# Kernel tuning notes

Hardware: AMD Instinct MI355X
Metric: run time of the kernel (lower is better)

The kernel has to match this reference:

```python
import jax, jax.numpy as jnp
import numpy as np

N, C, H, W = 64, 512, 16, 16
MEM_DIM, NUM_CLS = 2000, 10


def setup_inputs() -> dict:
    key = jax.random.key(0)
    k1, k2, k3 = jax.random.split(key, 3)
    z = jax.random.normal(k1, (N, C, H, W), dtype=jnp.float32)
    cls = jax.random.randint(k2, (N,), 0, NUM_CLS, dtype=jnp.int32)
    # nn.init.normal_(memory, 0.0, 0.02)
    memory = 0.02 * jax.random.normal(k3, (1, C, MEM_DIM, NUM_CLS), dtype=jnp.float32)
    return {"z": z, "cls": cls, "memory": memory}


def reference(z, cls, memory):
    n, c, h, w_ = z.shape
    hw = h * w_
    # memory[0,:,:,cls] -> (C, M, N) -> per-sample class memory (N, C, M)
    mem_cls = jnp.transpose(memory[0][:, :, cls], (2, 0, 1))  # (N, C, M)
    zf = z.reshape(n, c, hw)  # (N, C, HW)
    # similarity = -||z - m||^2 = 2 z.m - ||z||^2 - ||m||^2
    zm = jnp.einsum('ncp,ncm->npm', zf, mem_cls)          # (N, HW, M)
    z2 = jnp.sum(zf * zf, axis=1)[:, :, None]             # (N, HW, 1)
    m2 = jnp.sum(mem_cls * mem_cls, axis=1)[:, None, :]   # (N, 1, M)
    sim = 2.0 * zm - z2 - m2                               # (N, HW, M)
    log_w = jax.nn.log_softmax(sim, axis=2)
    w = jax.nn.softmax(sim, axis=2)
    w_hat = w  # topk == -1 in forward path
    # z_hat = bmm(mem_cls (N,C,M), w_hat^T (N,M,HW)) -> (N,C,HW)
    z_hat = jnp.einsum('ncm,npm->ncp', mem_cls, w_hat).reshape(n, c, h, w_)
    return (z_hat, w_hat, w, log_w)
```

## Files before the change

### kernel.cpp

```cpp
#include <hip/hip_runtime.h>
#include <hip/hip_bf16.h>
#include <math.h>

#define N_   64
#define C_   512
#define HW_  256
#define M_   2000
#define KCLS 10
#define MP_  2048

typedef __attribute__((ext_vector_type(8))) short bf16x8;
typedef __attribute__((ext_vector_type(4))) float f32x4;

__device__ __forceinline__ short f2bf(float x) {
    __hip_bfloat16 b = __float2bfloat16(x);
    return *reinterpret_cast<short*>(&b);
}
__device__ __forceinline__ float bf2f(short s) {
    __hip_bfloat16 b = *reinterpret_cast<__hip_bfloat16*>(&s);
    return __bfloat162float(b);
}

__global__ __launch_bounds__(256) void gather_mem(const float* __restrict__ mem,
                                                  short* __restrict__ mcm,
                                                  short* __restrict__ mmc) {
    const int m0 = blockIdx.x * 32;
    const int c0 = blockIdx.y * 64;
    __shared__ short tile[KCLS][32][66];
    const int t = threadIdx.x;
    const int mm = t & 31;
    const int m = m0 + mm;
    const int cbase = t >> 5;
    for (int ci = 0; ci < 8; ++ci) {
        const int cl = cbase + ci * 8;
        const int c = c0 + cl;
        short v[KCLS];
        if (m < M_) {
            const float* src = mem + ((size_t)c * M_ + m) * KCLS;
#pragma unroll
            for (int k = 0; k < KCLS; ++k) v[k] = f2bf(src[k]);
        } else {
#pragma unroll
            for (int k = 0; k < KCLS; ++k) v[k] = 0;
        }
#pragma unroll
        for (int k = 0; k < KCLS; ++k) {
            mcm[(size_t)k * (C_ * MP_) + (size_t)c * MP_ + m0 + mm] = v[k];
            tile[k][mm][cl] = v[k];
        }
    }
    __syncthreads();
    const int cc = t & 63;
    const int rbase = t >> 6;
    for (int k = 0; k < KCLS; ++k) {
#pragma unroll
        for (int r = 0; r < 8; ++r) {
            const int mm2 = r * 4 + rbase;
            mmc[(size_t)k * (MP_ * C_) + (size_t)(m0 + mm2) * C_ + c0 + cc] = tile[k][mm2][cc];
        }
    }
}

__global__ __launch_bounds__(256) void transpose_z(const float* __restrict__ z,
                                                   short* __restrict__ zTb) {
    const int c0 = blockIdx.x * 64;
    const int p0 = blockIdx.y * 64;
    const int n = blockIdx.z;
    const float* zp = z + (size_t)n * C_ * HW_;
    __shared__ short tile[64][70];
    const int t = threadIdx.x;
    const int pp = t & 63;
    const int cb = t >> 6;
#pragma unroll
    for (int i = 0; i < 16; ++i) {
        const int cl = i * 4 + cb;
        tile[cl][pp] = f2bf(zp[(size_t)(c0 + cl) * HW_ + p0 + pp]);
    }
    __syncthreads();
    short* dst = zTb + (size_t)n * HW_ * C_;
    const int cc = t & 63;
    const int pb = t >> 6;
#pragma unroll
    for (int i = 0; i < 16; ++i) {
        const int pl = i * 4 + pb;
        dst[(size_t)(p0 + pl) * C_ + c0 + cc] = tile[cc][pl];
    }
}

__global__ __launch_bounds__(256) void m2_kernel(const short* __restrict__ mcm,
                                                 float* __restrict__ m2) {
    const int m = blockIdx.x * 256 + threadIdx.x;
    const int k = blockIdx.y;
    if (m >= M_) return;
    const short* B = mcm + (size_t)k * C_ * MP_;
    float s = 0.f;
    for (int c = 0; c < C_; ++c) {
        float v = bf2f(B[(size_t)c * MP_ + m]);
        s = fmaf(v, v, s);
    }
    m2[k * M_ + m] = s;
}

template<int MODE>
__global__ __launch_bounds__(256) void gemm_nt(const short* __restrict__ Ab,
                                               const short* __restrict__ Bb,
                                               const float* __restrict__ Bf,
                                               const int* __restrict__ cls,
                                               const float* __restrict__ m2,
                                               float* __restrict__ Db) {
    constexpr int K  = (MODE == 0) ? C_ : MP_;
    constexpr int SA = (MODE == 0) ? C_ : MP_;
    constexpr int SB = (MODE == 0) ? C_ : MP_;
    const int bx = blockIdx.x, by = blockIdx.y, n = blockIdx.z;
    const int kc = cls[n];
    const int rowA0 = by * 128, colB0 = bx * 128;

    const short* A;
    const short* B  = nullptr;
    const float* BF = nullptr;
    float* D;
    if constexpr (MODE == 0) {
        A = Ab + (size_t)n * HW_ * C_;
        B = Bb + (size_t)kc * MP_ * C_;
        D = Db + (size_t)n * HW_ * M_;
    } else if constexpr (MODE == 1) {
        A = Ab + (size_t)kc * C_ * MP_;
        BF = Bf + (size_t)n * HW_ * M_;
        D = Db + (size_t)n * C_ * HW_;
    } else {
        A = Ab + (size_t)kc * C_ * MP_;
        B = Bb + (size_t)n * HW_ * MP_;
        D = Db + (size_t)n * C_ * HW_;
    }

    __shared__ short As[128 * 64];
    __shared__ short Bs[128 * 64];

    const int tid = threadIdx.x;
    const int w = tid >> 6, lane = tid & 63;
    const int wr = w >> 1, wc = w & 1;
    const int srow = lane >> 3, sslot = lane & 7;

    f32x4 acc[4][4];
#pragma unroll
    for (int i = 0; i < 4; ++i)
#pragma unroll
        for (int j = 0; j < 4; ++j) acc[i][j] = (f32x4){0.f, 0.f, 0.f, 0.f};

    for (int k0 = 0; k0 < K; k0 += 64) {
#pragma unroll
        for (int i = 0; i < 4; ++i) {
            const int row = w * 32 + i * 8 + srow;
            const int chunk = sslot ^ (row & 7);
            const short* src = A + (size_t)(rowA0 + row) * SA + k0 + chunk * 8;
            __builtin_amdgcn_global_load_lds(
                (const __attribute__((address_space(1))) void*)src,
                (__attribute__((address_space(3))) void*)&As[(w * 32 + i * 8) * 64],
                16, 0, 0);
        }
        if constexpr (MODE != 1) {
#pragma unroll
            for (int i = 0; i < 4; ++i) {
                const int row = w * 32 + i * 8 + srow;
                const int chunk = sslot ^ (row & 7);
                const short* src = B + (size_t)(colB0 + row) * SB + k0 + chunk * 8;
                __builtin_amdgcn_global_load_lds(
                    (const __attribute__((address_space(1))) void*)src,
                    (__attribute__((address_space(3))) void*)&Bs[(w * 32 + i * 8) * 64],
                    16, 0, 0);
            }
        } else {
#pragma unroll
            for (int i = 0; i < 4; ++i) {
                const int row = w * 32 + i * 8 + srow;
                const int kg = k0 + sslot * 8;
                float4 v0 = {0.f, 0.f, 0.f, 0.f}, v1 = {0.f, 0.f, 0.f, 0.f};
                if (kg < M_) {
                    const float* s = BF + (size_t)(colB0 + row) * M_ + kg;
                    v0 = *reinterpret_cast<const float4*>(s);
                    v1 = *reinterpret_cast<const float4*>(s + 4);
                }
                bf16x8 bv;
                bv[0] = f2bf(v0.x); bv[1] = f2bf(v0.y); bv[2] = f2bf(v0.z); bv[3] = f2bf(v0.w);
                bv[4] = f2bf(v1.x); bv[5] = f2bf(v1.y); bv[6] = f2bf(v1.z); bv[7] = f2bf(v1.w);
                *reinterpret_cast<bf16x8*>(&Bs[row * 64 + (sslot ^ (row & 7)) * 8]) = bv;
            }
        }
        __syncthreads();
        bf16x8 a[4][2], b[4][2];
#pragma unroll
        for (int i = 0; i < 4; ++i)
#pragma unroll
            for (int kk = 0; kk < 2; ++kk) {
                const int ra = wr * 64 + i * 16 + (lane & 15);
                const int slot = kk * 4 + (lane >> 4);
                a[i][kk] = *reinterpret_cast<const bf16x8*>(&As[ra * 64 + (slot ^ (ra & 7)) * 8]);
                const int rb = wc * 64 + i * 16 + (lane & 15);
                b[i][kk] = *reinterpret_cast<const bf16x8*>(&Bs[rb * 64 + (slot ^ (rb & 7)) * 8]);
            }
#pragma unroll
        for (int i = 0; i < 4; ++i)
#pragma unroll
            for (int j = 0; j < 4; ++j)
#pragma unroll
                for (int kk = 0; kk < 2; ++kk)
                    acc[i][j] = __builtin_amdgcn_mfma_f32_16x16x32_bf16(a[i][kk], b[j][kk], acc[i][j], 0, 0, 0);
        __syncthreads();
    }

    if constexpr (MODE == 0) {
#pragma unroll
        for (int j = 0; j < 4; ++j) {
            const int col = colB0 + wc * 64 + j * 16 + (lane & 15);
            if (col < M_) {
                const float m2v = m2[kc * M_ + col];
#pragma unroll
                for (int i = 0; i < 4; ++i) {
                    const int row = rowA0 + wr * 64 + i * 16 + (lane >> 4) * 4;
#pragma unroll
                    for (int r = 0; r < 4; ++r)
                        D[(size_t)(row + r) * M_ + col] = 2.f * acc[i][j][r] - m2v;
                }
            }
        }
    } else {
#pragma unroll
        for (int i = 0; i < 4; ++i) {
            const int row = rowA0 + wr * 64 + i * 16 + (lane >> 4) * 4;
#pragma unroll
            for (int j = 0; j < 4; ++j) {
                const int col = colB0 + wc * 64 + j * 16 + (lane & 15);
#pragma unroll
                for (int r = 0; r < 4; ++r)
                    D[(size_t)(row + r) * HW_ + col] = acc[i][j][r];
            }
        }
    }
}

__global__ __launch_bounds__(256) void softmax_kernel(const float* __restrict__ simbuf,
                                                      float* __restrict__ w_hat,
                                                      float* __restrict__ w,
                                                      float* __restrict__ logw,
                                                      short* __restrict__ wb,
                                                      int write_hat) {
    const int r = blockIdx.x;
    const float* srow = simbuf + (size_t)r * M_;
    const int t = threadIdx.x;

    float s0[8];
    float lmax = -INFINITY;
#pragma unroll
    for (int i = 0; i < 8; ++i) {
        int idx = t + i * 256;
        float x = (idx < M_) ? srow[idx] : -INFINITY;
        s0[i] = x;
        lmax = fmaxf(lmax, x);
    }
#pragma unroll
    for (int off = 32; off >= 1; off >>= 1)
        lmax = fmaxf(lmax, __shfl_xor(lmax, off));

    __shared__ float wred[4];
    __shared__ float wsum[4];
    const int wid = t >> 6, lane = t & 63;
    if (lane == 0) wred[wid] = lmax;
    __syncthreads();
    const float gmax = fmaxf(fmaxf(wred[0], wred[1]), fmaxf(wred[2], wred[3]));

    float e[8];
    float lsum = 0.f;
#pragma unroll
    for (int i = 0; i < 8; ++i) {
        int idx = t + i * 256;
        if (idx < M_) {
            e[i] = __expf(s0[i] - gmax);
            lsum += e[i];
        }
    }
#pragma unroll
    for (int off = 32; off >= 1; off >>= 1)
        lsum += __shfl_xor(lsum, off);
    if (lane == 0) wsum[wid] = lsum;
    __syncthreads();
    const float gsum = wsum[0] + wsum[1] + wsum[2] + wsum[3];
    const float inv = 1.f / gsum;
    const float lg  = __logf(gsum);

    size_t base = (size_t)r * M_;
    size_t base2 = (size_t)r * MP_;
#pragma unroll
    for (int i = 0; i < 8; ++i) {
        int idx = t + i * 256;
        if (idx < M_) {
            float wv = e[i] * inv;
            w[base + idx] = wv;
            if (write_hat) w_hat[base + idx] = wv;
            logw[base + idx] = (s0[i] - gmax) - lg;
            if (wb) wb[base2 + idx] = f2bf(wv);
        } else {
            if (wb) wb[base2 + idx] = 0;
        }
    }
}

__global__ __launch_bounds__(256) void copy_kernel(const float* __restrict__ src,
                                                   float* __restrict__ dst, int n4) {
    int i = blockIdx.x * 256 + threadIdx.x;
    int stride = gridDim.x * 256;
    for (; i < n4; i += stride)
        reinterpret_cast<float4*>(dst)[i] = reinterpret_cast<const float4*>(src)[i];
}

extern "C" void kernel_launch(void* const* d_in, const int* in_sizes, int n_in,
                              void* d_out, int out_size, void* d_ws, size_t ws_size,
                              hipStream_t stream) {
    const float* z      = (const float*)d_in[0];
    const int*   cls    = (const int*)d_in[1];
    const float* memory = (const float*)d_in[2];

    float* out   = (float*)d_out;
    float* z_hat = out;
    float* w_hat = z_hat + (size_t)N_ * C_ * HW_;
    float* w     = w_hat + (size_t)N_ * HW_ * M_;
    float* logw  = w     + (size_t)N_ * HW_ * M_;

    const size_t mcm_sh = (size_t)KCLS * C_ * MP_;
    const size_t mmc_sh = mcm_sh;
    const size_t zTb_sh = (size_t)N_ * HW_ * C_;
    const size_t wb_sh  = (size_t)N_ * HW_ * MP_;
    const size_t m2_fl  = (size_t)KCLS * M_;
    const size_t need_base = (mcm_sh + mmc_sh + zTb_sh) * 2 + m2_fl * 4;
    const size_t need_full = need_base + wb_sh * 2;

    short *mcm, *mmc, *zTb, *wb = nullptr;
    float* m2;
    int write_hat;
    if (ws_size >= need_base) {
        char* p = (char*)d_ws;
        mcm = (short*)p;          p += mcm_sh * 2;
        mmc = (short*)p;          p += mmc_sh * 2;
        m2  = (float*)p;          p += m2_fl * 4;
        zTb = (short*)p;          p += zTb_sh * 2;
        if (ws_size >= need_full) wb = (short*)p;
        write_hat = 1;
    } else {
        char* p = (char*)w_hat;
        mcm = (short*)p;          p += mcm_sh * 2;
        mmc = (short*)p;          p += mmc_sh * 2;
        m2  = (float*)p;
        zTb = (short*)z_hat;
        write_hat = 0;
    }
    float* simbuf = logw;

    gather_mem<<<dim3(MP_ / 32, C_ / 64), 256, 0, stream>>>(memory, mcm, mmc);
    transpose_z<<<dim3(C_ / 64, HW_ / 64, N_), 256, 0, stream>>>(z, zTb);
    m2_kernel<<<dim3(MP_ / 256, KCLS), 256, 0, stream>>>(mcm, m2);
    gemm_nt<0><<<dim3(MP_ / 128, HW_ / 128, N_), 256, 0, stream>>>(zTb, mmc, nullptr, cls, m2, simbuf);
    softmax_kernel<<<N_ * HW_, 256, 0, stream>>>(simbuf, w_hat, w, logw, wb, write_hat);
    if (wb)
        gemm_nt<2><<<dim3(HW_ / 128, C_ / 128, N_), 256, 0, stream>>>(mcm, wb, nullptr, cls, m2, z_hat);
    else
        gemm_nt<1><<<dim3(HW_ / 128, C_ / 128, N_), 256, 0, stream>>>(mcm, nullptr, w, cls, m2, z_hat);
    if (!write_hat)
        copy_kernel<<<2048, 256, 0, stream>>>(w, w_hat, (N_ * HW_ * M_) / 4);
}
```

Baseline: 308.4 us.

## Store similarity as bf16 via LDS-staged coalesced epilogues, remap blocks across XCDs

The similarity GEMM now writes its output as bf16 into a padded buffer (row stride 4000 shorts) through an LDS-staged, swizzled tile, so stores are 16-byte and coalesced. The softmax reads one 8-wide bf16 vector per thread and writes w, w_hat and log_w with float4 stores. The z_hat GEMM epilogue is also staged through LDS for float4 stores, and workgroups are remapped so consecutive logical tiles are spread across the 8 XCDs. This halves similarity traffic and removes scattered stores, at the cost of bf16 rounding of the logits before softmax and log_softmax, which may hurt accuracy.

After: 280.3 us. -9.1%, faster.

```diff
diff --git a/kernel.cpp b/kernel.cpp
--- a/kernel.cpp
+++ b/kernel.cpp
@@ -8,6 +8,7 @@
 #define M_   2000
 #define KCLS 10
 #define MP_  2048
+#define SIMS 4000
 
 typedef __attribute__((ext_vector_type(8))) short bf16x8;
 typedef __attribute__((ext_vector_type(4))) float f32x4;
@@ -91,14 +92,13 @@
                                                  float* __restrict__ m2) {
     const int m = blockIdx.x * 256 + threadIdx.x;
     const int k = blockIdx.y;
-    if (m >= M_) return;
     const short* B = mcm + (size_t)k * C_ * MP_;
     float s = 0.f;
     for (int c = 0; c < C_; ++c) {
         float v = bf2f(B[(size_t)c * MP_ + m]);
         s = fmaf(v, v, s);
     }
-    m2[k * M_ + m] = s;
+    m2[k * MP_ + m] = s;
 }
 
 template<int MODE>
@@ -111,30 +111,37 @@
     constexpr int K  = (MODE == 0) ? C_ : MP_;
     constexpr int SA = (MODE == 0) ? C_ : MP_;
     constexpr int SB = (MODE == 0) ? C_ : MP_;
-    const int bx = blockIdx.x, by = blockIdx.y, n = blockIdx.z;
+    constexpr int GX = (MODE == 0) ? 16 : 2;
+    constexpr int GY = (MODE == 0) ? 2 : 4;
+    constexpr int NWG = GX * GY * N_;
+    constexpr int CPX = NWG / 8;
+
+    const int flat = blockIdx.x + GX * (blockIdx.y + GY * blockIdx.z);
+    const int logical = (flat & 7) * CPX + (flat >> 3);
+    const int n  = logical / (GX * GY);
+    const int rr = logical % (GX * GY);
+    const int by = rr / GX, bx = rr % GX;
+
     const int kc = cls[n];
     const int rowA0 = by * 128, colB0 = bx * 128;
 
     const short* A;
     const short* B  = nullptr;
     const float* BF = nullptr;
-    float* D;
     if constexpr (MODE == 0) {
         A = Ab + (size_t)n * HW_ * C_;
         B = Bb + (size_t)kc * MP_ * C_;
-        D = Db + (size_t)n * HW_ * M_;
     } else if constexpr (MODE == 1) {
         A = Ab + (size_t)kc * C_ * MP_;
         BF = Bf + (size_t)n * HW_ * M_;
-        D = Db + (size_t)n * C_ * HW_;
     } else {
         A = Ab + (size_t)kc * C_ * MP_;
         B = Bb + (size_t)n * HW_ * MP_;
-        D = Db + (size_t)n * C_ * HW_;
-    }
-
-    __shared__ short As[128 * 64];
-    __shared__ short Bs[128 * 64];
+    }
+
+    __shared__ short smem[2 * 128 * 64];
+    short* As = smem;
+    short* Bs = smem + 128 * 64;
 
     const int tid = threadIdx.x;
     const int w = tid >> 6, lane = tid & 63;
@@ -209,54 +216,87 @@
     }
 
     if constexpr (MODE == 0) {
-#pragma unroll
-        for (int j = 0; j < 4; ++j) {
-            const int col = colB0 + wc * 64 + j * 16 + (lane & 15);
-            if (col < M_) {
-                const float m2v = m2[kc * M_ + col];
-#pragma unroll
-                for (int i = 0; i < 4; ++i) {
-                    const int row = rowA0 + wr * 64 + i * 16 + (lane >> 4) * 4;
-#pragma unroll
-                    for (int r = 0; r < 4; ++r)
-                        D[(size_t)(row + r) * M_ + col] = 2.f * acc[i][j][r] - m2v;
+        short* outs = smem;
+#pragma unroll
+        for (int i = 0; i < 4; ++i)
+#pragma unroll
+            for (int j = 0; j < 4; ++j) {
+                const int col = wc * 64 + j * 16 + (lane & 15);
+                const float m2v = m2[kc * MP_ + colB0 + col];
+#pragma unroll
+                for (int r = 0; r < 4; ++r) {
+                    const int row = wr * 64 + i * 16 + (lane >> 4) * 4 + r;
+                    outs[row * 128 + (col ^ (((row >> 2) & 7) << 3))] =
+                        f2bf(2.f * acc[i][j][r] - m2v);
                 }
             }
+        __syncthreads();
+        short* Ds = (short*)Db;
+        const size_t rbase = (size_t)n * HW_ + rowA0;
+#pragma unroll
+        for (int it = 0; it < 8; ++it) {
+            const int chunk = tid + it * 256;
+            const int row = chunk >> 4, c8 = (chunk & 15) * 8;
+            bf16x8 v = *reinterpret_cast<const bf16x8*>(
+                &outs[row * 128 + (c8 ^ (((row >> 2) & 7) << 3))]);
+            *reinterpret_cast<bf16x8*>(Ds + (rbase + row) * SIMS + colB0 + c8) = v;
         }
     } else {
-#pragma unroll
-        for (int i = 0; i < 4; ++i) {
-            const int row = rowA0 + wr * 64 + i * 16 + (lane >> 4) * 4;
-#pragma unroll
-            for (int j = 0; j < 4; ++j) {
-                const int col = colB0 + wc * 64 + j * 16 + (lane & 15);
-#pragma unroll
-                for (int r = 0; r < 4; ++r)
-                    D[(size_t)(row + r) * HW_ + col] = acc[i][j][r];
-            }
-        }
-    }
-}
-
-__global__ __launch_bounds__(256) void softmax_kernel(const float* __restrict__ simbuf,
+        float* outf = (float*)smem;
+        float* D = Db + (size_t)n * C_ * HW_;
+#pragma unroll
+        for (int h = 0; h < 2; ++h) {
+            if (wr == h) {
+#pragma unroll
+                for (int i = 0; i < 4; ++i)
+#pragma unroll
+                    for (int j = 0; j < 4; ++j) {
+                        const int col = wc * 64 + j * 16 + (lane & 15);
+#pragma unroll
+                        for (int r = 0; r < 4; ++r) {
+                            const int row = i * 16 + (lane >> 4) * 4 + r;
+                            outf[row * 128 + (col ^ (((row >> 2) & 1) << 4))] = acc[i][j][r];
+                        }
+                    }
+            }
+            __syncthreads();
+#pragma unroll
+            for (int it = 0; it < 8; ++it) {
+                const int chunk = tid + it * 256;
+                const int row = chunk >> 5, c4 = (chunk & 31) * 4;
+                float4 v = *reinterpret_cast<const float4*>(
+                    &outf[row * 128 + (c4 ^ (((row >> 2) & 1) << 4))]);
+                *reinterpret_cast<float4*>(
+                    &D[(size_t)(rowA0 + h * 64 + row) * HW_ + colB0 + c4]) = v;
+            }
+            __syncthreads();
+        }
+    }
+}
+
+__global__ __launch_bounds__(256) void softmax_kernel(const short* __restrict__ simb,
                                                       float* __restrict__ w_hat,
                                                       float* __restrict__ w,
                                                       float* __restrict__ logw,
                                                       short* __restrict__ wb,
                                                       int write_hat) {
     const int r = blockIdx.x;
-    const float* srow = simbuf + (size_t)r * M_;
     const int t = threadIdx.x;
-
-    float s0[8];
-    float lmax = -INFINITY;
-#pragma unroll
-    for (int i = 0; i < 8; ++i) {
-        int idx = t + i * 256;
-        float x = (idx < M_) ? srow[idx] : -INFINITY;
-        s0[i] = x;
-        lmax = fmaxf(lmax, x);
-    }
+    const bool valid = t < (M_ / 8);
+
+    float s[8];
+    if (valid) {
+        bf16x8 v = *reinterpret_cast<const bf16x8*>(simb + (size_t)r * SIMS + t * 8);
+#pragma unroll
+        for (int i = 0; i < 8; ++i) s[i] = bf2f(v[i]);
+    } else {
+#pragma unroll
+        for (int i = 0; i < 8; ++i) s[i] = -INFINITY;
+    }
+
+    float lmax = s[0];
+#pragma unroll
+    for (int i = 1; i < 8; ++i) lmax = fmaxf(lmax, s[i]);
 #pragma unroll
     for (int off = 32; off >= 1; off >>= 1)
         lmax = fmaxf(lmax, __shfl_xor(lmax, off));
@@ -270,11 +310,10 @@
 
     float e[8];
     float lsum = 0.f;
-#pragma unroll
-    for (int i = 0; i < 8; ++i) {
-        int idx = t + i * 256;
-        if (idx < M_) {
-            e[i] = __expf(s0[i] - gmax);
+    if (valid) {
+#pragma unroll
+        for (int i = 0; i < 8; ++i) {
+            e[i] = __expf(s[i] - gmax);
             lsum += e[i];
         }
     }
@@ -287,20 +326,32 @@
     const float inv = 1.f / gsum;
     const float lg  = __logf(gsum);
 
-    size_t base = (size_t)r * M_;
-    size_t base2 = (size_t)r * MP_;
-#pragma unroll
-    for (int i = 0; i < 8; ++i) {
-        int idx = t + i * 256;
-        if (idx < M_) {
-            float wv = e[i] * inv;
-            w[base + idx] = wv;
-            if (write_hat) w_hat[base + idx] = wv;
-            logw[base + idx] = (s0[i] - gmax) - lg;
-            if (wb) wb[base2 + idx] = f2bf(wv);
-        } else {
-            if (wb) wb[base2 + idx] = 0;
-        }
+    if (valid) {
+        const size_t base = (size_t)r * M_ + t * 8;
+        float4 w0, w1, l0, l1;
+        w0.x = e[0] * inv; w0.y = e[1] * inv; w0.z = e[2] * inv; w0.w = e[3] * inv;
+        w1.x = e[4] * inv; w1.y = e[5] * inv; w1.z = e[6] * inv; w1.w = e[7] * inv;
+        l0.x = s[0] - gmax - lg; l0.y = s[1] - gmax - lg;
+        l0.z = s[2] - gmax - lg; l0.w = s[3] - gmax - lg;
+        l1.x = s[4] - gmax - lg; l1.y = s[5] - gmax - lg;
+        l1.z = s[6] - gmax - lg; l1.w = s[7] - gmax - lg;
+        *reinterpret_cast<float4*>(w + base)     = w0;
+        *reinterpret_cast<float4*>(w + base + 4) = w1;
+        if (write_hat) {
+            *reinterpret_cast<float4*>(w_hat + base)     = w0;
+            *reinterpret_cast<float4*>(w_hat + base + 4) = w1;
+        }
+        *reinterpret_cast<float4*>(logw + base)     = l0;
+        *reinterpret_cast<float4*>(logw + base + 4) = l1;
+        if (wb) {
+            bf16x8 bv;
+            bv[0] = f2bf(w0.x); bv[1] = f2bf(w0.y); bv[2] = f2bf(w0.z); bv[3] = f2bf(w0.w);
+            bv[4] = f2bf(w1.x); bv[5] = f2bf(w1.y); bv[6] = f2bf(w1.z); bv[7] = f2bf(w1.w);
+            *reinterpret_cast<bf16x8*>(wb + (size_t)r * MP_ + t * 8) = bv;
+        }
+    } else if (wb) {
+        bf16x8 zv = {0, 0, 0, 0, 0, 0, 0, 0};
+        *reinterpret_cast<bf16x8*>(wb + (size_t)r * MP_ + t * 8) = zv;
     }
 }
 
@@ -329,7 +380,7 @@
     const size_t mmc_sh = mcm_sh;
     const size_t zTb_sh = (size_t)N_ * HW_ * C_;
     const size_t wb_sh  = (size_t)N_ * HW_ * MP_;
-    const size_t m2_fl  = (size_t)KCLS * M_;
+    const size_t m2_fl  = (size_t)KCLS * MP_;
     const size_t need_base = (mcm_sh + mmc_sh + zTb_sh) * 2 + m2_fl * 4;
     const size_t need_full = need_base + wb_sh * 2;
 
@@ -352,17 +403,17 @@
         zTb = (short*)z_hat;
         write_hat = 0;
     }
-    float* simbuf = logw;
+    short* simb = (short*)logw;
 
     gather_mem<<<dim3(MP_ / 32, C_ / 64), 256, 0, stream>>>(memory, mcm, mmc);
     transpose_z<<<dim3(C_ / 64, HW_ / 64, N_), 256, 0, stream>>>(z, zTb);
     m2_kernel<<<dim3(MP_ / 256, KCLS), 256, 0, stream>>>(mcm, m2);
-    gemm_nt<0><<<dim3(MP_ / 128, HW_ / 128, N_), 256, 0, stream>>>(zTb, mmc, nullptr, cls, m2, simbuf);
-    softmax_kernel<<<N_ * HW_, 256, 0, stream>>>(simbuf, w_hat, w, logw, wb, write_hat);
+    gemm_nt<0><<<dim3(16, 2, N_), 256, 0, stream>>>(zTb, mmc, nullptr, cls, m2, logw);
+    softmax_kernel<<<N_ * HW_, 256, 0, stream>>>(simb, w_hat, w, logw, wb, write_hat);
     if (wb)
-        gemm_nt<2><<<dim3(HW_ / 128, C_ / 128, N_), 256, 0, stream>>>(mcm, wb, nullptr, cls, m2, z_hat);
+        gemm_nt<2><<<dim3(2, 4, N_), 256, 0, stream>>>(mcm, wb, nullptr, cls, m2, z_hat);
     else
-        gemm_nt<1><<<dim3(HW_ / 128, C_ / 128, N_), 256, 0, stream>>>(mcm, nullptr, w, cls, m2, z_hat);
+        gemm_nt<1><<<dim3(2, 4, N_), 256, 0, stream>>>(mcm, nullptr, w, cls, m2, z_hat);
     if (!write_hat)
         copy_kernel<<<2048, 256, 0, stream>>>(w, w_hat, (N_ * HW_ * M_) / 4);
 }
```
